# Kernel optimization log

Hardware: AMD Instinct MI355X
Metric: run time of the kernel (lower is better)

## Reference

```python
import jax, jax.numpy as jnp
import numpy as np

EPS = 1e-5
H = 8
D_HEAD = 64


def feature_norm(x, gamma, beta):
    # Normalizes over the sequence dim (dim=1), matching the torch module.
    mean = x.mean(axis=1, keepdims=True)
    var = x.var(axis=1, keepdims=True)  # unbiased=False == population var
    return gamma * (x - mean) / jnp.sqrt(var + EPS) + beta


def swish(x):
    return x * jax.nn.sigmoid(x)


def setup_inputs() -> dict:
    key = jax.random.key(0)
    B, N, D = 8, 1024, 256
    d_expand, d_time = 1024, 256
    d_q = D_HEAD * H          # 512
    d_v = D * H               # 2048
    d_qkv = 2 * d_q + d_v     # 3072
    ks = jax.random.split(key, 10)
    s = 0.02
    return {
        "x": jax.random.normal(ks[0], (B, N, D), jnp.float32),
        "t": jax.random.normal(ks[1], (B, 1, d_time), jnp.float32),
        "gamma": jnp.ones((1, 1, D), jnp.float32),
        "beta": jnp.zeros((1, 1, D), jnp.float32),
        "pos_enc": jax.random.normal(ks[2], (1, N, D), jnp.float32) * 0.02,
        "Wqkv": jax.random.normal(ks[3], (D, d_qkv), jnp.float32) * s,
        "bqkv": jnp.zeros((d_qkv,), jnp.float32),
        "Wm": jax.random.normal(ks[4], (D * H, D), jnp.float32) * s,
        "bm": jnp.zeros((D,), jnp.float32),
        "Wt": jax.random.normal(ks[5], (d_time, D + d_expand), jnp.float32) * s,
        "bt": jnp.zeros((D + d_expand,), jnp.float32),
        "gamma1": jnp.ones((1, 1, D), jnp.float32),
        "beta1": jnp.zeros((1, 1, D), jnp.float32),
        "Wf1": jax.random.normal(ks[6], (D, d_expand), jnp.float32) * s,
        "bf1": jnp.zeros((d_expand,), jnp.float32),
        "Wf2": jax.random.normal(ks[7], (d_expand, D), jnp.float32) * s,
        "bf2": jnp.zeros((D,), jnp.float32),
        "scale": jnp.float32(1.414),
    }


def reference(x, t, gamma, beta, pos_enc, Wqkv, bqkv, Wm, bm, Wt, bt,
              gamma1, beta1, Wf1, bf1, Wf2, bf2, scale):
    B, N, D = x.shape
    d_q = D_HEAD * H
    # qkv projection with Swish pre-activation
    h = swish(feature_norm(x, gamma, beta) + pos_enc)
    qkv = h @ Wqkv + bqkv                              # [B,N,2*d_q + D*H]
    q, k, v = jnp.split(qkv, [d_q, 2 * d_q], axis=-1)
    q = q.reshape(B, N, H, D_HEAD).transpose(0, 2, 1, 3)   # [B,H,N,Dh]
    k = k.reshape(B, N, H, D_HEAD).transpose(0, 2, 1, 3)
    v = v.reshape(B, N, H, D).transpose(0, 2, 1, 3)        # [B,H,N,D]
    # Gaussian-kernel attention: exp(-||q-k||^2 / scale^2), no softmax
    q2 = jnp.sum(q * q, axis=-1)                           # [B,H,N]
    k2 = jnp.sum(k * k, axis=-1)                           # [B,H,N]
    d2 = q2[..., :, None] + k2[..., None, :] - 2.0 * jnp.einsum('bhnc,bhmc->bhnm', q, k)
    attn = jnp.exp(-jnp.maximum(d2, 0.0) / (scale * scale))  # [B,H,N,N]
    out = jnp.einsum('bhnm,bhmc->bhnc', attn, v)           # [B,H,N,D]
    out = out.transpose(0, 2, 1, 3).reshape(B, N, H * D)   # B N (H C)
    x = x + out @ Wm + bm
    # time-conditioned FFN
    ts = t @ Wt + bt                                       # [B,1,D+d_expand]
    t_shift, t_scale = jnp.split(ts, [D], axis=-1)
    ff = swish(feature_norm(x + t_shift, gamma1, beta1)) @ Wf1 + bf1
    ff = swish(ff * jax.nn.sigmoid(t_scale))
    return ff @ Wf2 + bf2 + x  # shortcut is Identity (d_in == d_out)
```

## Files before the change

### kernel.cpp

```cpp
#include <hip/hip_runtime.h>
#include <math.h>

typedef __attribute__((ext_vector_type(4))) float f32x4;
typedef __attribute__((ext_vector_type(16))) float f32x16;
typedef __attribute__((ext_vector_type(8))) short short8;

#define DI __device__ __forceinline__

static constexpr int Bb = 8;
static constexpr int Nn = 1024;
static constexpr int Dd = 256;

DI unsigned short f2bf(float f) {
  union { float f; unsigned u; } v; v.f = f;
  unsigned r = v.u + 0x7fffu + ((v.u >> 16) & 1u);
  return (unsigned short)(r >> 16);
}
DI float bf2f(unsigned short h) {
  union { unsigned u; float f; } v; v.u = ((unsigned)h) << 16; return v.f;
}

DI void gload_lds16(const void* g, void* l) {
  __builtin_amdgcn_global_load_lds((const __attribute__((address_space(1))) unsigned int*)g,
                                   (__attribute__((address_space(3))) unsigned int*)l, 16, 0, 0);
}

__global__ void stats_pass1(const float* __restrict__ x, float* __restrict__ partial) {
  int d = threadIdx.x;
  int b = blockIdx.x >> 5;
  int c = blockIdx.x & 31;
  const float* p = x + ((size_t)b * Nn + c * 32) * Dd + d;
  float s = 0.f, ss = 0.f;
  for (int i = 0; i < 32; i++) { float v = p[(size_t)i * Dd]; s += v; ss += v * v; }
  float* o = partial + ((size_t)(b * 32 + c) * 2) * Dd + d;
  o[0] = s; o[Dd] = ss;
}

__global__ void stats_pass2(const float* __restrict__ partial, float* __restrict__ mean,
                            float* __restrict__ rstd) {
  int d = threadIdx.x; int b = blockIdx.x;
  float s = 0.f, ss = 0.f;
  for (int c = 0; c < 32; c++) {
    s  += partial[((size_t)(b * 32 + c) * 2) * Dd + d];
    ss += partial[((size_t)(b * 32 + c) * 2) * Dd + Dd + d];
  }
  float m = s * (1.f / Nn);
  float var = ss * (1.f / Nn) - m * m;
  mean[b * Dd + d] = m;
  rstd[b * Dd + d] = rsqrtf(var + 1e-5f);
}

template<bool POS>
__global__ void norm_swish(const float* __restrict__ x, const float* __restrict__ mean,
                           const float* __restrict__ rstd, const float* __restrict__ gamma,
                           const float* __restrict__ beta, const float* __restrict__ pos,
                           unsigned short* __restrict__ out) {
  size_t idx = ((size_t)blockIdx.x * 256 + threadIdx.x) * 4;
  int d = (int)(idx & (Dd - 1));
  size_t row = idx >> 8;
  int b = (int)(row >> 10);
  int n = (int)(row & (Nn - 1));
  const float4 xv = *(const float4*)(x + idx);
  const float4 gv = *(const float4*)(gamma + d);
  const float4 bv = *(const float4*)(beta + d);
  const float4 mv = *(const float4*)(mean + b * Dd + d);
  const float4 rv = *(const float4*)(rstd + b * Dd + d);
  float v[4]  = {xv.x, xv.y, xv.z, xv.w};
  float g[4]  = {gv.x, gv.y, gv.z, gv.w};
  float be[4] = {bv.x, bv.y, bv.z, bv.w};
  float mm[4] = {mv.x, mv.y, mv.z, mv.w};
  float rr[4] = {rv.x, rv.y, rv.z, rv.w};
  float pp[4] = {0.f, 0.f, 0.f, 0.f};
  if (POS) {
    const float4 pv = *(const float4*)(pos + (size_t)n * Dd + d);
    pp[0] = pv.x; pp[1] = pv.y; pp[2] = pv.z; pp[3] = pv.w;
  }
  ushort4 o;
  unsigned short* op = (unsigned short*)&o;
  #pragma unroll
  for (int j = 0; j < 4; j++) {
    float val = (v[j] - mm[j]) * rr[j] * g[j] + be[j];
    if (POS) val += pp[j];
    float sw = val / (1.f + __expf(-val));
    op[j] = f2bf(sw);
  }
  *(ushort4*)(out + idx) = o;
}

__global__ void time_proj(const float* __restrict__ t, const float* __restrict__ Wt,
                          const float* __restrict__ bt, float* __restrict__ sig_ts) {
  int j = blockIdx.x * 256 + threadIdx.x;
  int b = blockIdx.y;
  const float* tb = t + b * 256;
  float acc = bt[256 + j];
  for (int k = 0; k < 256; k++) acc += tb[k] * Wt[k * 1280 + 256 + j];
  sig_ts[b * 1024 + j] = 1.f / (1.f + __expf(-acc));
}

__global__ void transpose_w(const float* __restrict__ in, unsigned short* __restrict__ out,
                            int R, int C) {
  __shared__ float tile[32][33];
  int c0 = blockIdx.x * 32, r0 = blockIdx.y * 32;
  int tx = threadIdx.x & 31, ty = threadIdx.x >> 5;
  for (int i = ty; i < 32; i += 8)
    tile[i][tx] = in[(size_t)(r0 + i) * C + c0 + tx];
  __syncthreads();
  for (int i = ty; i < 32; i += 8)
    out[(size_t)(c0 + i) * R + r0 + tx] = f2bf(tile[tx][i]);
}

template<int EPI, int BN>
__global__ __launch_bounds__(256, 3) void gemm2(
    const unsigned short* __restrict__ A, const unsigned short* __restrict__ BT,
    const float* __restrict__ bias, const float* __restrict__ res,
    const float* __restrict__ aux, unsigned short* __restrict__ obf,
    float* __restrict__ of, unsigned short* __restrict__ vtb, int K, int Ndim) {
  __shared__ __align__(16) unsigned short As[128 * 64];
  __shared__ __align__(16) unsigned short Bs[BN * 64];
  const int tid = threadIdx.x, lane = tid & 63, wave = tid >> 6;
  const int wr = wave >> 1, wc = wave & 1;
  constexpr int NI = (BN == 128) ? 4 : 2;
  constexpr int WCW = (BN == 128) ? 64 : 32;
  const int m0 = blockIdx.y * 128, n0 = blockIdx.x * BN;
  f32x4 acc[4][NI] = {};
  for (int k0 = 0; k0 < K; k0 += 64) {
    __syncthreads();
    #pragma unroll
    for (int p = 0; p < 4; p++) {
      const int o = p * 4096 + tid * 16;
      const int row = o >> 7, c8 = (o >> 4) & 7;
      gload_lds16(A + (size_t)(m0 + row) * K + k0 + c8 * 8, (char*)As + o);
    }
    #pragma unroll
    for (int p = 0; p < BN / 32; p++) {
      const int o = p * 4096 + tid * 16;
      const int row = o >> 7, c8 = (o >> 4) & 7;
      gload_lds16(BT + (size_t)(n0 + row) * K + k0 + c8 * 8, (char*)Bs + o);
    }
    __syncthreads();
    #pragma unroll
    for (int ks = 0; ks < 2; ks++) {
      short8 af[4], bfr[NI];
      #pragma unroll
      for (int i = 0; i < 4; i++)
        af[i] = *(const short8*)&As[(wr * 64 + i * 16 + (lane & 15)) * 64 + ks * 32 + (lane >> 4) * 8];
      #pragma unroll
      for (int i = 0; i < NI; i++)
        bfr[i] = *(const short8*)&Bs[(wc * WCW + i * 16 + (lane & 15)) * 64 + ks * 32 + (lane >> 4) * 8];
      #pragma unroll
      for (int mi = 0; mi < 4; mi++)
        #pragma unroll
        for (int ni = 0; ni < NI; ni++)
          acc[mi][ni] = __builtin_amdgcn_mfma_f32_16x16x32_bf16(af[mi], bfr[ni], acc[mi][ni], 0, 0, 0);
    }
  }
  const int rbase = m0 + wr * 64 + ((lane >> 4) << 2);
  const int cb = n0 + wc * WCW + (lane & 15);
  #pragma unroll
  for (int mi = 0; mi < 4; mi++) {
    #pragma unroll
    for (int ni = 0; ni < NI; ni++) {
      const int col = cb + ni * 16;
      const float bv = bias[col];
      const int r0_ = rbase + mi * 16;
      if (EPI == 0) {
        if (col < 1024) {
          #pragma unroll
          for (int j = 0; j < 4; j++)
            obf[(size_t)(r0_ + j) * 1024 + col] = f2bf(acc[mi][ni][j] + bv);
        } else {
          const int hh = (col - 1024) >> 8, cc = (col - 1024) & 255;
          const int b_ = r0_ >> 10, nb = r0_ & (Nn - 1);
          ushort4 pk;
          unsigned short* pp = (unsigned short*)&pk;
          #pragma unroll
          for (int j = 0; j < 4; j++) pp[j] = f2bf(acc[mi][ni][j] + bv);
          *(ushort4*)&vtb[((size_t)((b_ * 8 + hh) * 256 + cc)) * 1024 + nb] = pk;
        }
      } else if (EPI == 1) {
        #pragma unroll
        for (int j = 0; j < 4; j++) {
          size_t o = (size_t)(r0_ + j) * Ndim + col;
          of[o] = acc[mi][ni][j] + bv + res[o];
        }
      } else {
        const int b_ = r0_ >> 10;
        const float sg = aux[b_ * 1024 + col];
        #pragma unroll
        for (int j = 0; j < 4; j++) {
          float g = (acc[mi][ni][j] + bv) * sg;
          obf[(size_t)(r0_ + j) * Ndim + col] = f2bf(g / (1.f + __expf(-g)));
        }
      }
    }
  }
}

__global__ __launch_bounds__(512, 2) void attn2(
    const unsigned short* __restrict__ qk, const unsigned short* __restrict__ vt,
    unsigned short* __restrict__ aout, const float* __restrict__ scale_p) {
  const int dd = blockIdx.x;
  const int bh = (dd & 7) + ((dd >> 5) << 3);
  const int qt = (dd >> 3) & 3;
  const int b = bh >> 3, h = bh & 7;
  const float sc = scale_p[0];
  const float inv_s2 = 1.f / (sc * sc);

  __shared__ __align__(16) unsigned short Ks[2][64 * 64];
  __shared__ __align__(16) unsigned short Vs[2][256 * 64];
  __shared__ __align__(16) unsigned short Ps[256 * 64];
  __shared__ __align__(16) float k2w[8][32];

  const int tid = threadIdx.x, lane = tid & 63, wave = tid >> 6;
  const int qg = wave >> 1, cg = wave & 1;
  const int l31 = lane & 31, lh = lane >> 5;

  auto stage = [&](int kt, int buf) {
    {
      const int row = tid >> 3;
      const int c8 = (tid & 7) ^ (row & 7);
      gload_lds16(qk + (size_t)(b * 1024 + kt * 64 + row) * 1024 + 512 + h * 64 + c8 * 8,
                  (char*)&Ks[buf][0] + tid * 16);
    }
    #pragma unroll
    for (int p = 0; p < 4; p++) {
      const int o = p * 8192 + tid * 16;
      const int row = o >> 7;
      const int c8 = ((o >> 4) & 7) ^ (row & 7);
      gload_lds16(vt + (size_t)(bh * 256 + row) * 1024 + kt * 64 + c8 * 8,
                  (char*)&Vs[buf][0] + o);
    }
  };

  stage(0, 0);

  short8 qfrag[2][4];
  float q2r[2];
  const unsigned short* qbase = qk + (size_t)(b * 1024 + qt * 256 + qg * 64) * 1024 + h * 64;
  #pragma unroll
  for (int qc = 0; qc < 2; qc++) {
    float s = 0.f;
    #pragma unroll
    for (int ks = 0; ks < 4; ks++) {
      short8 v = *(const short8*)(qbase + (size_t)(qc * 32 + l31) * 1024 + ks * 16 + lh * 8);
      qfrag[qc][ks] = v;
      #pragma unroll
      for (int j = 0; j < 8; j++) { float f = bf2f(((unsigned short*)&v)[j]); s += f * f; }
    }
    s += __shfl_xor(s, 32);
    q2r[qc] = s;
  }

  f32x16 acc[2][4] = {};
  __syncthreads();

  for (int kt = 0; kt < 16; kt++) {
    const int cur = kt & 1;
    if (kt < 15) stage(kt + 1, cur ^ 1);

    {
      const int r = lane >> 1, half = lane & 1;
      const int row = cg * 32 + r;
      float s = 0.f;
      #pragma unroll
      for (int i = 0; i < 4; i++) {
        const int sl = (half * 4 + i) ^ (row & 7);
        short8 v = *(const short8*)((const char*)&Ks[cur][0] + row * 128 + sl * 16);
        #pragma unroll
        for (int j = 0; j < 8; j++) { float f = bf2f(((unsigned short*)&v)[j]); s += f * f; }
      }
      s += __shfl_xor(s, 1);
      if (half == 0) k2w[wave][r] = s;
    }

    short8 kf[4];
    #pragma unroll
    for (int ks = 0; ks < 4; ks++) {
      const int row = cg * 32 + l31;
      const int sl = (ks * 2 + lh) ^ (row & 7);
      kf[ks] = *(const short8*)((const char*)&Ks[cur][0] + row * 128 + sl * 16);
    }
    float4 k2q[4];
    #pragma unroll
    for (int g = 0; g < 4; g++) k2q[g] = *(const float4*)&k2w[wave][lh * 4 + g * 8];

    #pragma unroll
    for (int qc = 0; qc < 2; qc++) {
      f32x16 sacc = {};
      #pragma unroll
      for (int ks = 0; ks < 4; ks++)
        sacc = __builtin_amdgcn_mfma_f32_32x32x16_bf16(kf[ks], qfrag[qc][ks], sacc, 0, 0, 0);
      const int row = qg * 64 + qc * 32 + l31;
      const int rsw = (row & 7) << 4;
      #pragma unroll
      for (int g = 0; g < 4; g++) {
        ushort4 pk;
        #pragma unroll
        for (int j = 0; j < 4; j++) {
          float d2 = q2r[qc] + ((const float*)&k2q[g])[j] - 2.f * sacc[g * 4 + j];
          float pv = __expf(-fmaxf(d2, 0.f) * inv_s2);
          ((unsigned short*)&pk)[j] = f2bf(pv);
        }
        const int kbyte = cg * 64 + g * 16 + lh * 8;
        *(ushort4*)((char*)Ps + row * 128 + (kbyte ^ rsw)) = pk;
      }
    }
    __syncthreads();

    #pragma unroll
    for (int ks = 0; ks < 4; ks++) {
      short8 pf[2];
      #pragma unroll
      for (int mi = 0; mi < 2; mi++) {
        const int row = qg * 64 + mi * 32 + l31;
        const int sl = (ks * 2 + lh) ^ (row & 7);
        pf[mi] = *(const short8*)((const char*)Ps + row * 128 + sl * 16);
      }
      #pragma unroll
      for (int ci = 0; ci < 4; ci++) {
        const int vrow = cg * 128 + ci * 32 + l31;
        const int sl = (ks * 2 + lh) ^ (vrow & 7);
        short8 vf = *(const short8*)((const char*)&Vs[cur][0] + vrow * 128 + sl * 16);
        #pragma unroll
        for (int mi = 0; mi < 2; mi++)
          acc[mi][ci] = __builtin_amdgcn_mfma_f32_32x32x16_bf16(pf[mi], vf, acc[mi][ci], 0, 0, 0);
      }
    }
    __syncthreads();
  }

  const size_t row0 = (size_t)(b * 1024 + qt * 256 + qg * 64);
  #pragma unroll
  for (int mi = 0; mi < 2; mi++)
    #pragma unroll
    for (int ci = 0; ci < 4; ci++) {
      #pragma unroll
      for (int r = 0; r < 16; r++) {
        const int q = mi * 32 + (r & 3) + 8 * (r >> 2) + 4 * lh;
        const int c = h * 256 + cg * 128 + ci * 32 + l31;
        aout[(row0 + q) * 2048 + c] = f2bf(acc[mi][ci][r]);
      }
    }
}

extern "C" void kernel_launch(void* const* d_in, const int* in_sizes, int n_in,
                              void* d_out, int out_size, void* d_ws, size_t ws_size,
                              hipStream_t stream) {
  (void)in_sizes; (void)n_in; (void)out_size; (void)ws_size;
  const float* x      = (const float*)d_in[0];
  const float* t      = (const float*)d_in[1];
  const float* gamma  = (const float*)d_in[2];
  const float* beta   = (const float*)d_in[3];
  const float* pos    = (const float*)d_in[4];
  const float* Wqkv   = (const float*)d_in[5];
  const float* bqkv   = (const float*)d_in[6];
  const float* Wm     = (const float*)d_in[7];
  const float* bm     = (const float*)d_in[8];
  const float* Wt     = (const float*)d_in[9];
  const float* bt     = (const float*)d_in[10];
  const float* gamma1 = (const float*)d_in[11];
  const float* beta1  = (const float*)d_in[12];
  const float* Wf1    = (const float*)d_in[13];
  const float* bf1    = (const float*)d_in[14];
  const float* Wf2    = (const float*)d_in[15];
  const float* bf2    = (const float*)d_in[16];
  const float* scale  = (const float*)d_in[17];
  float* out = (float*)d_out;

  char* ws = (char*)d_ws;
  size_t off = 0;
  auto alloc = [&](size_t bytes) -> void* {
    void* p = ws + off;
    off += (bytes + 255) & ~(size_t)255;
    return p;
  };
  unsigned short* qkb   = (unsigned short*)alloc((size_t)8192 * 1024 * 2);
  unsigned short* vtb   = (unsigned short*)alloc((size_t)64 * 256 * 1024 * 2);
  unsigned short* aoutb = (unsigned short*)alloc((size_t)8192 * 2048 * 2);
  unsigned short* hbuf  = (unsigned short*)alloc((size_t)8192 * 256 * 2);
  unsigned short* ffbuf = (unsigned short*)alloc((size_t)8192 * 1024 * 2);
  float* x1             = (float*)alloc((size_t)8192 * 256 * 4);
  unsigned short* WqkvT = (unsigned short*)alloc((size_t)3072 * 256 * 2);
  unsigned short* WmT   = (unsigned short*)alloc((size_t)256 * 2048 * 2);
  unsigned short* Wf1T  = (unsigned short*)alloc((size_t)1024 * 256 * 2);
  unsigned short* Wf2T  = (unsigned short*)alloc((size_t)256 * 1024 * 2);
  float* partial = (float*)alloc((size_t)8 * 32 * 2 * 256 * 4);
  float* mean1   = (float*)alloc(8 * 256 * 4);
  float* rstd1   = (float*)alloc(8 * 256 * 4);
  float* mean2   = (float*)alloc(8 * 256 * 4);
  float* rstd2   = (float*)alloc(8 * 256 * 4);
  float* sig_ts  = (float*)alloc(8 * 1024 * 4);

  transpose_w<<<dim3(96, 8),  256, 0, stream>>>(Wqkv, WqkvT, 256, 3072);
  transpose_w<<<dim3(8, 64),  256, 0, stream>>>(Wm,   WmT,   2048, 256);
  transpose_w<<<dim3(32, 8),  256, 0, stream>>>(Wf1,  Wf1T,  256, 1024);
  transpose_w<<<dim3(8, 32),  256, 0, stream>>>(Wf2,  Wf2T,  1024, 256);

  stats_pass1<<<256, 256, 0, stream>>>(x, partial);
  stats_pass2<<<8, 256, 0, stream>>>(partial, mean1, rstd1);
  time_proj<<<dim3(4, 8), 256, 0, stream>>>(t, Wt, bt, sig_ts);
  norm_swish<true><<<2048, 256, 0, stream>>>(x, mean1, rstd1, gamma, beta, pos, hbuf);

  gemm2<0, 128><<<dim3(24, 64), 256, 0, stream>>>(hbuf, WqkvT, bqkv, nullptr, nullptr,
                                                  qkb, nullptr, vtb, 256, 3072);
  attn2<<<256, 512, 0, stream>>>(qkb, vtb, aoutb, scale);
  gemm2<1, 64><<<dim3(4, 64), 256, 0, stream>>>(aoutb, WmT, bm, x, nullptr,
                                                nullptr, x1, nullptr, 2048, 256);

  stats_pass1<<<256, 256, 0, stream>>>(x1, partial);
  stats_pass2<<<8, 256, 0, stream>>>(partial, mean2, rstd2);
  norm_swish<false><<<2048, 256, 0, stream>>>(x1, mean2, rstd2, gamma1, beta1, nullptr, hbuf);

  gemm2<2, 128><<<dim3(8, 64), 256, 0, stream>>>(hbuf, Wf1T, bf1, nullptr, sig_ts,
                                                 ffbuf, nullptr, nullptr, 256, 1024);
  gemm2<1, 64><<<dim3(4, 64), 256, 0, stream>>>(ffbuf, Wf2T, bf2, x1, nullptr,
                                                nullptr, out, nullptr, 1024, 256);
}
```

Baseline: 212.7 us.

## Keep attention probabilities in registers and precompute query/key norms

The attention kernel is restructured so each wave owns 32 query rows across all 256 value columns. The exp probabilities are packed to bf16 with v_cvt_pk_bf16_f32 and rearranged across lane halves with v_permlane32_swap, then fed straight into the PV MFMA as the A operand. This removes the shared-memory P buffer and one barrier per key tile. The squared norms of q and k move into a separate small kernel that writes them to global memory, so the per-tile k2 reduction in LDS goes away. In exchange there is an extra kernel launch, more accumulator registers per wave (8 f32x16), and repeated K fragment loads per wave.

```diff
diff --git a/kernel.cpp b/kernel.cpp
--- a/kernel.cpp
+++ b/kernel.cpp
@@ -107,6 +107,27 @@
   __syncthreads();
   for (int i = ty; i < 32; i += 8)
     out[(size_t)(c0 + i) * R + r0 + tx] = f2bf(tile[tx][i]);
+}
+
+__global__ void q2k2_kernel(const unsigned short* __restrict__ qk,
+                            float* __restrict__ q2, float* __restrict__ k2) {
+  const int wave = threadIdx.x >> 6, lane = threadIdx.x & 63;
+  const int r = blockIdx.x * 4 + wave;
+  const int b = r >> 10, n = r & 1023;
+  short8 v = *(const short8*)(qk + (size_t)r * 1024 + lane * 16);
+  float s = 0.f;
+  #pragma unroll
+  for (int j = 0; j < 8; j++) { float f = bf2f(((unsigned short*)&v)[j]); s += f * f; }
+  short8 v2 = *(const short8*)(qk + (size_t)r * 1024 + lane * 16 + 8);
+  #pragma unroll
+  for (int j = 0; j < 8; j++) { float f = bf2f(((unsigned short*)&v2)[j]); s += f * f; }
+  s += __shfl_xor(s, 1);
+  s += __shfl_xor(s, 2);
+  if ((lane & 3) == 0) {
+    const int seg = lane >> 2;
+    float* dst = (seg < 8) ? q2 : k2;
+    dst[(size_t)(b * 8 + (seg & 7)) * 1024 + n] = s;
+  }
 }
 
 template<int EPI, int BN>
@@ -196,8 +217,9 @@
   }
 }
 
-__global__ __launch_bounds__(512, 2) void attn2(
+__global__ __launch_bounds__(512, 2) void attn3(
     const unsigned short* __restrict__ qk, const unsigned short* __restrict__ vt,
+    const float* __restrict__ q2g, const float* __restrict__ k2g,
     unsigned short* __restrict__ aout, const float* __restrict__ scale_p) {
   const int dd = blockIdx.x;
   const int bh = (dd & 7) + ((dd >> 5) << 3);
@@ -208,12 +230,10 @@
 
   __shared__ __align__(16) unsigned short Ks[2][64 * 64];
   __shared__ __align__(16) unsigned short Vs[2][256 * 64];
-  __shared__ __align__(16) unsigned short Ps[256 * 64];
-  __shared__ __align__(16) float k2w[8][32];
 
   const int tid = threadIdx.x, lane = tid & 63, wave = tid >> 6;
-  const int qg = wave >> 1, cg = wave & 1;
   const int l31 = lane & 31, lh = lane >> 5;
+  const int qr0 = qt * 256 + wave * 32;
 
   auto stage = [&](int kt, int buf) {
     {
@@ -234,113 +254,78 @@
 
   stage(0, 0);
 
-  short8 qfrag[2][4];
-  float q2r[2];
-  const unsigned short* qbase = qk + (size_t)(b * 1024 + qt * 256 + qg * 64) * 1024 + h * 64;
-  #pragma unroll
-  for (int qc = 0; qc < 2; qc++) {
-    float s = 0.f;
-    #pragma unroll
-    for (int ks = 0; ks < 4; ks++) {
-      short8 v = *(const short8*)(qbase + (size_t)(qc * 32 + l31) * 1024 + ks * 16 + lh * 8);
-      qfrag[qc][ks] = v;
-      #pragma unroll
-      for (int j = 0; j < 8; j++) { float f = bf2f(((unsigned short*)&v)[j]); s += f * f; }
-    }
-    s += __shfl_xor(s, 32);
-    q2r[qc] = s;
-  }
-
-  f32x16 acc[2][4] = {};
+  short8 qfrag[4];
+  const unsigned short* qbase = qk + (size_t)(b * 1024 + qr0 + l31) * 1024 + h * 64;
+  #pragma unroll
+  for (int ks = 0; ks < 4; ks++)
+    qfrag[ks] = *(const short8*)(qbase + ks * 16 + lh * 8);
+  const float q2v = q2g[(size_t)bh * 1024 + qr0 + l31];
+
+  f32x16 acc[8] = {};
   __syncthreads();
 
   for (int kt = 0; kt < 16; kt++) {
     const int cur = kt & 1;
     if (kt < 15) stage(kt + 1, cur ^ 1);
 
-    {
-      const int r = lane >> 1, half = lane & 1;
-      const int row = cg * 32 + r;
-      float s = 0.f;
-      #pragma unroll
-      for (int i = 0; i < 4; i++) {
-        const int sl = (half * 4 + i) ^ (row & 7);
-        short8 v = *(const short8*)((const char*)&Ks[cur][0] + row * 128 + sl * 16);
-        #pragma unroll
-        for (int j = 0; j < 8; j++) { float f = bf2f(((unsigned short*)&v)[j]); s += f * f; }
+    uint4 pa[4];
+    #pragma unroll
+    for (int mi = 0; mi < 2; mi++) {
+      f32x16 sacc = {};
+      #pragma unroll
+      for (int ks = 0; ks < 4; ks++) {
+        const int row = mi * 32 + l31;
+        const int sl = (ks * 2 + lh) ^ (row & 7);
+        short8 kf = *(const short8*)((const char*)&Ks[cur][0] + row * 128 + sl * 16);
+        sacc = __builtin_amdgcn_mfma_f32_32x32x16_bf16(kf, qfrag[ks], sacc, 0, 0, 0);
       }
-      s += __shfl_xor(s, 1);
-      if (half == 0) k2w[wave][r] = s;
-    }
-
-    short8 kf[4];
-    #pragma unroll
-    for (int ks = 0; ks < 4; ks++) {
-      const int row = cg * 32 + l31;
-      const int sl = (ks * 2 + lh) ^ (row & 7);
-      kf[ks] = *(const short8*)((const char*)&Ks[cur][0] + row * 128 + sl * 16);
-    }
-    float4 k2q[4];
-    #pragma unroll
-    for (int g = 0; g < 4; g++) k2q[g] = *(const float4*)&k2w[wave][lh * 4 + g * 8];
-
-    #pragma unroll
-    for (int qc = 0; qc < 2; qc++) {
-      f32x16 sacc = {};
-      #pragma unroll
-      for (int ks = 0; ks < 4; ks++)
-        sacc = __builtin_amdgcn_mfma_f32_32x32x16_bf16(kf[ks], qfrag[qc][ks], sacc, 0, 0, 0);
-      const int row = qg * 64 + qc * 32 + l31;
-      const int rsw = (row & 7) << 4;
+      const float* k2p = k2g + (size_t)bh * 1024 + kt * 64 + mi * 32 + lh * 4;
+      float pr[16];
       #pragma unroll
       for (int g = 0; g < 4; g++) {
-        ushort4 pk;
+        const float4 k2v = *(const float4*)(k2p + g * 8);
         #pragma unroll
         for (int j = 0; j < 4; j++) {
-          float d2 = q2r[qc] + ((const float*)&k2q[g])[j] - 2.f * sacc[g * 4 + j];
-          float pv = __expf(-fmaxf(d2, 0.f) * inv_s2);
-          ((unsigned short*)&pk)[j] = f2bf(pv);
+          float d2 = q2v + ((const float*)&k2v)[j] - 2.f * sacc[g * 4 + j];
+          pr[g * 4 + j] = __expf(-fmaxf(d2, 0.f) * inv_s2);
         }
-        const int kbyte = cg * 64 + g * 16 + lh * 8;
-        *(ushort4*)((char*)Ps + row * 128 + (kbyte ^ rsw)) = pk;
       }
+      #pragma unroll
+      for (int ksh = 0; ksh < 2; ksh++) {
+        unsigned w0, w1, w2, w3;
+        const int o = ksh * 8;
+        asm("v_cvt_pk_bf16_f32 %0, %1, %2" : "=v"(w0) : "v"(pr[o + 0]), "v"(pr[o + 1]));
+        asm("v_cvt_pk_bf16_f32 %0, %1, %2" : "=v"(w1) : "v"(pr[o + 2]), "v"(pr[o + 3]));
+        asm("v_cvt_pk_bf16_f32 %0, %1, %2" : "=v"(w2) : "v"(pr[o + 4]), "v"(pr[o + 5]));
+        asm("v_cvt_pk_bf16_f32 %0, %1, %2" : "=v"(w3) : "v"(pr[o + 6]), "v"(pr[o + 7]));
+        asm("v_permlane32_swap_b32 %0, %1" : "+v"(w0), "+v"(w2));
+        asm("v_permlane32_swap_b32 %0, %1" : "+v"(w1), "+v"(w3));
+        pa[mi * 2 + ksh] = make_uint4(w0, w1, w2, w3);
+      }
+    }
+    #pragma unroll
+    for (int ci = 0; ci < 8; ci++) {
+      #pragma unroll
+      for (int ks = 0; ks < 4; ks++) {
+        const int row = ci * 32 + l31;
+        const int sl = (ks * 2 + lh) ^ (row & 7);
+        short8 vf = *(const short8*)((const char*)&Vs[cur][0] + row * 128 + sl * 16);
+        short8 paf = *(const short8*)&pa[ks];
+        acc[ci] = __builtin_amdgcn_mfma_f32_32x32x16_bf16(paf, vf, acc[ci], 0, 0, 0);
+      }
     }
     __syncthreads();
-
-    #pragma unroll
-    for (int ks = 0; ks < 4; ks++) {
-      short8 pf[2];
-      #pragma unroll
-      for (int mi = 0; mi < 2; mi++) {
-        const int row = qg * 64 + mi * 32 + l31;
-        const int sl = (ks * 2 + lh) ^ (row & 7);
-        pf[mi] = *(const short8*)((const char*)Ps + row * 128 + sl * 16);
-      }
-      #pragma unroll
-      for (int ci = 0; ci < 4; ci++) {
-        const int vrow = cg * 128 + ci * 32 + l31;
-        const int sl = (ks * 2 + lh) ^ (vrow & 7);
-        short8 vf = *(const short8*)((const char*)&Vs[cur][0] + vrow * 128 + sl * 16);
-        #pragma unroll
-        for (int mi = 0; mi < 2; mi++)
-          acc[mi][ci] = __builtin_amdgcn_mfma_f32_32x32x16_bf16(pf[mi], vf, acc[mi][ci], 0, 0, 0);
-      }
-    }
-    __syncthreads();
-  }
-
-  const size_t row0 = (size_t)(b * 1024 + qt * 256 + qg * 64);
-  #pragma unroll
-  for (int mi = 0; mi < 2; mi++)
-    #pragma unroll
-    for (int ci = 0; ci < 4; ci++) {
-      #pragma unroll
-      for (int r = 0; r < 16; r++) {
-        const int q = mi * 32 + (r & 3) + 8 * (r >> 2) + 4 * lh;
-        const int c = h * 256 + cg * 128 + ci * 32 + l31;
-        aout[(row0 + q) * 2048 + c] = f2bf(acc[mi][ci][r]);
-      }
-    }
+  }
+
+  const size_t row0 = (size_t)(b * 1024 + qr0);
+  #pragma unroll
+  for (int ci = 0; ci < 8; ci++) {
+    #pragma unroll
+    for (int r = 0; r < 16; r++) {
+      const int q = (r & 3) + 8 * (r >> 2) + 4 * lh;
+      aout[(row0 + q) * 2048 + h * 256 + ci * 32 + l31] = f2bf(acc[ci][r]);
+    }
+  }
 }
 
 extern "C" void kernel_launch(void* const* d_in, const int* in_sizes, int n_in,
@@ -390,6 +375,8 @@
   float* mean2   = (float*)alloc(8 * 256 * 4);
   float* rstd2   = (float*)alloc(8 * 256 * 4);
   float* sig_ts  = (float*)alloc(8 * 1024 * 4);
+  float* q2g     = (float*)alloc((size_t)64 * 1024 * 4);
+  float* k2g     = (float*)alloc((size_t)64 * 1024 * 4);
 
   transpose_w<<<dim3(96, 8),  256, 0, stream>>>(Wqkv, WqkvT, 256, 3072);
   transpose_w<<<dim3(8, 64),  256, 0, stream>>>(Wm,   WmT,   2048, 256);
@@ -403,7 +390,8 @@
 
   gemm2<0, 128><<<dim3(24, 64), 256, 0, stream>>>(hbuf, WqkvT, bqkv, nullptr, nullptr,
                                                   qkb, nullptr, vtb, 256, 3072);
-  attn2<<<256, 512, 0, stream>>>(qkb, vtb, aoutb, scale);
+  q2k2_kernel<<<2048, 256, 0, stream>>>(qkb, q2g, k2g);
+  attn3<<<256, 512, 0, stream>>>(qkb, vtb, q2g, k2g, aoutb, scale);
   gemm2<1, 64><<<dim3(4, 64), 256, 0, stream>>>(aoutb, WmT, bm, x, nullptr,
                                                 nullptr, x1, nullptr, 2048, 256);
 
```

New measurement: 206.9 us. 2.7% less time.
